# Kernel tuning notes

Measured on AMD Instinct MI355X. Metric: run time of the kernel, lower is better.

The kernel has to match this reference:

```python
import jax, jax.numpy as jnp
from jax import lax
import numpy as np

EPS = 1e-8


def _pdist(a):
    # torch.cdist(a, a, p=2): pairwise Euclidean distances [B, B]
    sq = jnp.sum(a * a, axis=1)
    d2 = sq[:, None] + sq[None, :] - 2.0 * (a @ a.T)
    d2 = jnp.maximum(d2, 0.0)
    # safe sqrt: zero distance -> 0 with zero (not NaN) gradient
    pos = d2 > 0
    return jnp.where(pos, jnp.sqrt(jnp.where(pos, d2, 1.0)), 0.0)


def _local_curvature(x, k):
    # PCA-residual curvature per sample: 1 - S0 / sum(S) over k-NN neighborhood
    dists = _pdist(x)                          # [B, B]
    _, knn_idx = lax.top_k(-dists, k + 1)      # smallest k+1 distances
    knn_idx = knn_idx[:, 1:]                   # drop self -> [B, k]
    nbrs = x[knn_idx]                          # [B, k, D] gather
    centered = nbrs - jnp.mean(nbrs, axis=1, keepdims=True)
    S = jnp.linalg.svd(centered, compute_uv=False)  # batched singular values [B, k]
    linearity = S[:, 0] / (jnp.sum(S, axis=1) + EPS)
    return 1.0 - linearity                     # [B]


def reference(z, ref_emb, x_original, k):
    B = z.shape[0]
    curv = _local_curvature(x_original, k)     # [B]
    z_dist = _pdist(z)
    ref_dist = _pdist(ref_emb)
    # weights = clamp(1 - max(curv_i, curv_j), min=0.1)
    weights = jnp.maximum(1.0 - jnp.maximum(curv[:, None], curv[None, :]), 0.1)
    z_norm = z_dist / (jnp.max(z_dist) + EPS)
    ref_norm = ref_dist / (jnp.max(ref_dist) + EPS)
    errors = (z_norm - ref_norm) ** 2 * weights
    mask = jnp.triu(jnp.ones((B, B), dtype=bool), k=1)
    n_pairs = B * (B - 1) / 2.0
    return jnp.sum(jnp.where(mask, errors, 0.0)) / n_pairs


def setup_inputs() -> dict:
    key = jax.random.key(0)
    k1, k2, k3 = jax.random.split(key, 3)
    B, D, DZ, DR = 4096, 1024, 128, 128
    return {
        "z": jax.random.normal(k1, (B, DZ), dtype=jnp.float32),
        "ref_emb": jax.random.normal(k2, (B, DR), dtype=jnp.float32),
        "x_original": jax.random.normal(k3, (B, D), dtype=jnp.float32),
        "k": 10,
    }
```

## Files before the change

### kernel.cpp

```cpp
#include <hip/hip_runtime.h>
#include <math.h>

#define NB 4096
#define DX 1024
#define DZ 128
#define KNN 10
#define STR 32
#define NLIST 32
#define BKK 64

typedef short short8v __attribute__((ext_vector_type(8)));
typedef float f32x4 __attribute__((ext_vector_type(4)));

#define MFMA16(a, b, c) __builtin_amdgcn_mfma_f32_16x16x32_bf16((a), (b), (c), 0, 0, 0)

__device__ __forceinline__ ushort f2bf(float f) {
  unsigned u = __float_as_uint(f);
  u += 0x7FFFu + ((u >> 16) & 1u);
  return (ushort)(u >> 16);
}
__device__ __forceinline__ float bf2f(ushort h) {
  return __uint_as_float(((unsigned)h) << 16);
}

__device__ __forceinline__ short8v frag_ld(const ushort* base, int row, int fg) {
  int off = (row << 6) + (fg << 4);
  off ^= (row & 7) << 4;
  return *(const short8v*)((const char*)base + off);
}

__device__ __forceinline__ int swz64(int row, int c8) {
  return (row << 7) + ((c8 ^ (row & 7)) << 4);
}
__device__ __forceinline__ short8v frag_ld64(const ushort* base, int row, int kk, int fg) {
  return *(const short8v*)((const char*)base + swz64(row, kk * 4 + fg));
}

#define INSERT10(td, ti, v, idx)                         \
  do {                                                   \
    if ((v) < td[KNN - 1]) {                             \
      _Pragma("unroll")                                  \
      for (int k_ = KNN - 1; k_ >= 1; --k_) {            \
        bool bk = (v) < td[k_];                          \
        bool bk1 = (v) < td[k_ - 1];                     \
        td[k_] = bk ? (bk1 ? td[k_ - 1] : (v)) : td[k_]; \
        ti[k_] = bk ? (bk1 ? ti[k_ - 1] : (idx)) : ti[k_]; \
      }                                                  \
      bool b0 = (v) < td[0];                             \
      ti[0] = b0 ? (idx) : ti[0];                        \
      td[0] = b0 ? (v) : td[0];                          \
    }                                                    \
  } while (0)

__global__ __launch_bounds__(256) void k_rowsq(const float* __restrict__ a,
                                               float* __restrict__ out, int D) {
  int row = blockIdx.x;
  const float4* p = (const float4*)(a + (size_t)row * D);
  float s = 0.f;
  for (int d = threadIdx.x; d < (D >> 2); d += 256) {
    float4 v = p[d];
    s = fmaf(v.x, v.x, s); s = fmaf(v.y, v.y, s);
    s = fmaf(v.z, v.z, s); s = fmaf(v.w, v.w, s);
  }
#pragma unroll
  for (int m = 32; m; m >>= 1) s += __shfl_xor(s, m);
  __shared__ float red[4];
  int w = threadIdx.x >> 6;
  if ((threadIdx.x & 63) == 0) red[w] = s;
  __syncthreads();
  if (threadIdx.x == 0) out[row] = red[0] + red[1] + red[2] + red[3];
}

__global__ __launch_bounds__(256) void k_prep_x(const float* __restrict__ x,
                                                ushort* __restrict__ xh,
                                                float* __restrict__ sqx) {
  const int row = blockIdx.x, t = threadIdx.x;
  float4 v = ((const float4*)(x + (size_t)row * DX))[t];
  ushort4 hv;
  hv.x = f2bf(v.x); hv.y = f2bf(v.y); hv.z = f2bf(v.z); hv.w = f2bf(v.w);
  ((ushort4*)(xh + (size_t)row * DX))[t] = hv;
  float s = fmaf(v.x, v.x, fmaf(v.y, v.y, fmaf(v.z, v.z, v.w * v.w)));
#pragma unroll
  for (int m = 32; m; m >>= 1) s += __shfl_xor(s, m);
  __shared__ float red[4];
  int w = t >> 6;
  if ((t & 63) == 0) red[w] = s;
  __syncthreads();
  if (t == 0) sqx[row] = red[0] + red[1] + red[2] + red[3];
}

__global__ __launch_bounds__(256) void k_prep_zr(const float* __restrict__ z,
                                                 const float* __restrict__ rfm,
                                                 ushort* __restrict__ zh, ushort* __restrict__ zl,
                                                 ushort* __restrict__ rh, ushort* __restrict__ rl,
                                                 float* __restrict__ sqz, float* __restrict__ sqr) {
  const float* src = blockIdx.y ? rfm : z;
  ushort* ph = blockIdx.y ? rh : zh;
  ushort* pl = blockIdx.y ? rl : zl;
  float* sq = blockIdx.y ? sqr : sqz;
  const int t = threadIdx.x;
  const size_t base = (size_t)blockIdx.x * 1024;
  float4 v = ((const float4*)(src + base))[t];
  float vv[4] = {v.x, v.y, v.z, v.w};
  ushort h[4], l[4];
#pragma unroll
  for (int e = 0; e < 4; ++e) {
    h[e] = f2bf(vv[e]);
    l[e] = f2bf(vv[e] - bf2f(h[e]));
  }
  ushort4 hv; hv.x = h[0]; hv.y = h[1]; hv.z = h[2]; hv.w = h[3];
  ushort4 lv; lv.x = l[0]; lv.y = l[1]; lv.z = l[2]; lv.w = l[3];
  ((ushort4*)(ph + base))[t] = hv;
  ((ushort4*)(pl + base))[t] = lv;
  float s = fmaf(v.x, v.x, fmaf(v.y, v.y, fmaf(v.z, v.z, v.w * v.w)));
#pragma unroll
  for (int m = 16; m; m >>= 1) s += __shfl_xor(s, m);
  if ((t & 31) == 0) sq[blockIdx.x * 8 + (t >> 5)] = s;
}

struct SmemKNN {
  union {
    struct { ushort A[256 * BKK], B[128 * BKK]; } s;
    float D[64 * 129];
  } u;
};

template<int PRE>
__global__ __launch_bounds__(512, 4) void k_knn(const float* __restrict__ x,
                                                const ushort* __restrict__ xh,
                                                const float* __restrict__ sqx,
                                                float* __restrict__ cand_d,
                                                int* __restrict__ cand_i) {
  __shared__ SmemKNN sm;
  const int bid = blockIdx.y * STR + blockIdx.x;
  const int xcd = bid & 7, rr = bid >> 3;
  const int strip = (xcd & 3) * 8 + (rr & 7);
  const int itile = (xcd >> 2) * 8 + (rr >> 3);
  const int i0 = itile * 256;
  const int j0 = strip * 128;

  const int tid = threadIdx.x;
  const int lane = tid & 63, wv = tid >> 6;
  const int wr = wv >> 1, wc = wv & 1;
  const int fr = lane & 15, fg = lane >> 4;

  float td[KNN];
  int ti[KNN];
#pragma unroll
  for (int k = 0; k < KNN; ++k) { td[k] = 3.0e38f; ti[k] = 0; }
  const int my_chunk = tid >> 7;
  const int t2 = tid & 127;
  const int srow = t2 >> 1;
  const int cbase = (tid & 1) * 64;

  f32x4 acc[4][4];
  const f32x4 zv4 = {0.f, 0.f, 0.f, 0.f};
#pragma unroll
  for (int m = 0; m < 4; ++m)
#pragma unroll
    for (int n = 0; n < 4; ++n) acc[m][n] = zv4;

  for (int kc = 0; kc < DX; kc += BKK) {
    __syncthreads();
    if (PRE) {
#pragma unroll
      for (int l = 0; l < 4; ++l) {
        int idx = tid + l * 512;
        int row = idx >> 3, c8 = idx & 7;
        *(uint4*)((char*)sm.u.s.A + swz64(row, c8)) =
            *(const uint4*)(xh + (size_t)(i0 + row) * DX + kc + c8 * 8);
      }
#pragma unroll
      for (int l = 0; l < 2; ++l) {
        int idx = tid + l * 512;
        int row = idx >> 3, c8 = idx & 7;
        *(uint4*)((char*)sm.u.s.B + swz64(row, c8)) =
            *(const uint4*)(xh + (size_t)(j0 + row) * DX + kc + c8 * 8);
      }
    } else {
#pragma unroll
      for (int l = 0; l < 4; ++l) {
        int idx = tid + l * 512;
        int row = idx >> 3, c8 = idx & 7;
        const float* pa = &x[(size_t)(i0 + row) * DX + kc + c8 * 8];
        float4 a1 = *(const float4*)pa, a2 = *(const float4*)(pa + 4);
        uint4 pva;
        pva.x = (unsigned)f2bf(a1.x) | ((unsigned)f2bf(a1.y) << 16);
        pva.y = (unsigned)f2bf(a1.z) | ((unsigned)f2bf(a1.w) << 16);
        pva.z = (unsigned)f2bf(a2.x) | ((unsigned)f2bf(a2.y) << 16);
        pva.w = (unsigned)f2bf(a2.z) | ((unsigned)f2bf(a2.w) << 16);
        *(uint4*)((char*)sm.u.s.A + swz64(row, c8)) = pva;
      }
#pragma unroll
      for (int l = 0; l < 2; ++l) {
        int idx = tid + l * 512;
        int row = idx >> 3, c8 = idx & 7;
        const float* pb = &x[(size_t)(j0 + row) * DX + kc + c8 * 8];
        float4 b1 = *(const float4*)pb, b2 = *(const float4*)(pb + 4);
        uint4 pvb;
        pvb.x = (unsigned)f2bf(b1.x) | ((unsigned)f2bf(b1.y) << 16);
        pvb.y = (unsigned)f2bf(b1.z) | ((unsigned)f2bf(b1.w) << 16);
        pvb.z = (unsigned)f2bf(b2.x) | ((unsigned)f2bf(b2.y) << 16);
        pvb.w = (unsigned)f2bf(b2.z) | ((unsigned)f2bf(b2.w) << 16);
        *(uint4*)((char*)sm.u.s.B + swz64(row, c8)) = pvb;
      }
    }
    __syncthreads();
#pragma unroll
    for (int kk = 0; kk < 2; ++kk) {
      short8v fa[4];
#pragma unroll
      for (int m = 0; m < 4; ++m)
        fa[m] = frag_ld64(sm.u.s.A, wr * 64 + m * 16 + fr, kk, fg);
#pragma unroll
      for (int n = 0; n < 4; ++n) {
        short8v fb = frag_ld64(sm.u.s.B, wc * 64 + n * 16 + fr, kk, fg);
#pragma unroll
        for (int m = 0; m < 4; ++m)
          acc[m][n] = MFMA16(fa[m], fb, acc[m][n]);
      }
    }
  }
  __syncthreads();
#pragma unroll
  for (int chunk = 0; chunk < 4; ++chunk) {
    if (wr == chunk) {
#pragma unroll
      for (int m = 0; m < 4; ++m)
#pragma unroll
        for (int n = 0; n < 4; ++n)
#pragma unroll
          for (int r = 0; r < 4; ++r) {
            int rl = m * 16 + fg * 4 + r;
            int cl = wc * 64 + n * 16 + fr;
            int gi = i0 + chunk * 64 + rl, gj = j0 + cl;
            float v = sqx[gi] + sqx[gj] - 2.f * acc[m][n][r];
            sm.u.D[rl * 129 + cl] = (gi == gj) ? 3.0e38f : v;
          }
    }
    __syncthreads();
    if (my_chunk == chunk) {
#pragma unroll 4
      for (int c = 0; c < 64; ++c) {
        float v = sm.u.D[srow * 129 + cbase + c];
        int idx = j0 + cbase + c;
        INSERT10(td, ti, v, idx);
      }
    }
    __syncthreads();
  }
  {
    float pd[KNN]; int pi[KNN];
#pragma unroll
    for (int l = 0; l < KNN; ++l) {
      pd[l] = __shfl_xor(td[l], 1);
      pi[l] = __shfl_xor(ti[l], 1);
    }
#pragma unroll
    for (int l = 0; l < KNN; ++l) INSERT10(td, ti, pd[l], pi[l]);
    if ((tid & 1) == 0) {
      int row = i0 + my_chunk * 64 + srow;
#pragma unroll
      for (int l = 0; l < KNN; ++l) {
        cand_d[((size_t)row * NLIST + strip) * KNN + l] = td[l];
        cand_i[((size_t)row * NLIST + strip) * KNN + l] = ti[l];
      }
    }
  }
}

template<int PRE>
__global__ __launch_bounds__(64) void k_mergegram(const float* __restrict__ cand_d,
                                                  const int* __restrict__ cand_i,
                                                  const float* __restrict__ x,
                                                  const ushort* __restrict__ xh,
                                                  float* __restrict__ G) {
  const int pt = blockIdx.x;
  const int lane = threadIdx.x;
  float v[KNN]; int jx[KNN];
  const float* cd = cand_d + ((size_t)pt * NLIST + lane) * KNN;
  const int* ci = cand_i + ((size_t)pt * NLIST + lane) * KNN;
  const bool act = lane < NLIST;
#pragma unroll
  for (int l = 0; l < KNN; ++l) {
    v[l] = act ? cd[l] : 3.0e38f;
    jx[l] = act ? ci[l] : 0;
  }
  int nbi[KNN];
#pragma unroll
  for (int k = 0; k < KNN; ++k) {
    float bv = v[0]; int bj = jx[0]; int bl = lane;
#pragma unroll
    for (int m = 1; m < 64; m <<= 1) {
      float ov = __shfl_xor(bv, m);
      int oj = __shfl_xor(bj, m);
      int ol = __shfl_xor(bl, m);
      bool take = ov < bv;
      bv = take ? ov : bv; bj = take ? oj : bj; bl = take ? ol : bl;
    }
    nbi[k] = bj;
    if (lane == bl) {
#pragma unroll
      for (int l = 0; l < KNN - 1; ++l) { v[l] = v[l + 1]; jx[l] = jx[l + 1]; }
      v[KNN - 1] = 3.0e38f;
    }
  }
  float P[55];
  float U[KNN];
  float q = 0.f;
#pragma unroll
  for (int c = 0; c < 55; ++c) P[c] = 0.f;
#pragma unroll
  for (int a = 0; a < KNN; ++a) U[a] = 0.f;
  if (PRE) {
    const short8v* nb[KNN];
#pragma unroll
    for (int a = 0; a < KNN; ++a)
      nb[a] = (const short8v*)(xh + (size_t)nbi[a] * DX);
    for (int d8 = lane; d8 < DX / 8; d8 += 64) {
      short8v n8[KNN];
#pragma unroll
      for (int a = 0; a < KNN; ++a) n8[a] = nb[a][d8];
#pragma unroll
      for (int e = 0; e < 8; ++e) {
        float n[KNN];
#pragma unroll
        for (int a = 0; a < KNN; ++a) n[a] = bf2f((ushort)n8[a][e]);
        float m = 0.f;
#pragma unroll
        for (int a = 0; a < KNN; ++a) m += n[a];
        m *= 0.1f;
        q = fmaf(m, m, q);
#pragma unroll
        for (int a = 0; a < KNN; ++a) U[a] = fmaf(n[a], m, U[a]);
        int c = 0;
#pragma unroll
        for (int a = 0; a < KNN; ++a)
#pragma unroll
          for (int b = a; b < KNN; ++b) { P[c] = fmaf(n[a], n[b], P[c]); ++c; }
      }
    }
  } else {
    const float4* nb[KNN];
#pragma unroll
    for (int a = 0; a < KNN; ++a)
      nb[a] = (const float4*)(x + (size_t)nbi[a] * DX);
    for (int d4 = lane; d4 < DX / 4; d4 += 64) {
      float4 n4[KNN];
#pragma unroll
      for (int a = 0; a < KNN; ++a) n4[a] = nb[a][d4];
#pragma unroll
      for (int e = 0; e < 4; ++e) {
        float n[KNN];
#pragma unroll
        for (int a = 0; a < KNN; ++a) n[a] = ((const float*)&n4[a])[e];
        float m = 0.f;
#pragma unroll
        for (int a = 0; a < KNN; ++a) m += n[a];
        m *= 0.1f;
        q = fmaf(m, m, q);
#pragma unroll
        for (int a = 0; a < KNN; ++a) U[a] = fmaf(n[a], m, U[a]);
        int c = 0;
#pragma unroll
        for (int a = 0; a < KNN; ++a)
#pragma unroll
          for (int b = a; b < KNN; ++b) { P[c] = fmaf(n[a], n[b], P[c]); ++c; }
      }
    }
  }
#pragma unroll
  for (int c = 0; c < 55; ++c)
#pragma unroll
    for (int m2 = 32; m2; m2 >>= 1) P[c] += __shfl_xor(P[c], m2);
#pragma unroll
  for (int a = 0; a < KNN; ++a)
#pragma unroll
    for (int m2 = 32; m2; m2 >>= 1) U[a] += __shfl_xor(U[a], m2);
#pragma unroll
  for (int m2 = 32; m2; m2 >>= 1) q += __shfl_xor(q, m2);
  if (lane == 0) {
    int c = 0;
    for (int a = 0; a < KNN; ++a)
      for (int b = a; b < KNN; ++b) { G[(size_t)pt * 55 + c] = P[c] - U[a] - U[b] + q; ++c; }
  }
}

__device__ __forceinline__ constexpr int IJ(int a, int b) {
  return (a <= b) ? (10 * a - (a * (a - 1)) / 2 + (b - a))
                  : (10 * b - (b * (b - 1)) / 2 + (a - b));
}

#define NSWEEP 6
__global__ __launch_bounds__(64) void k_jacobi(const float* __restrict__ G,
                                               float* __restrict__ curv) {
  const int pt = blockIdx.x * 64 + threadIdx.x;
  float M[55];
#pragma unroll
  for (int c = 0; c < 55; ++c) M[c] = G[(size_t)pt * 55 + c];

#pragma unroll
  for (int sweep = 0; sweep < NSWEEP; ++sweep) {
#pragma unroll
    for (int p = 0; p < KNN - 1; ++p) {
#pragma unroll
      for (int q = p + 1; q < KNN; ++q) {
        float apq = M[IJ(p, q)];
        float app = M[IJ(p, p)], aqq = M[IJ(q, q)];
        float theta = (aqq - app) / (2.f * apq);
        float t = 1.f / (fabsf(theta) + sqrtf(fmaf(theta, theta, 1.f)));
        t = (theta < 0.f) ? -t : t;
        t = (apq == 0.f) ? 0.f : t;
        float cc = 1.f / sqrtf(fmaf(t, t, 1.f));
        float ss = t * cc;
#pragma unroll
        for (int r = 0; r < KNN; ++r) {
          if (r == p || r == q) continue;
          float vrp = M[IJ(r, p)];
          float vrq = M[IJ(r, q)];
          M[IJ(r, p)] = cc * vrp - ss * vrq;
          M[IJ(r, q)] = ss * vrp + cc * vrq;
        }
        M[IJ(p, p)] = app - t * apq;
        M[IJ(q, q)] = aqq + t * apq;
        M[IJ(p, q)] = 0.f;
      }
    }
  }

  float lmax = 0.f, ssum = 0.f;
#pragma unroll
  for (int a = 0; a < KNN; ++a) {
    float l = fmaxf(M[IJ(a, a)], 0.f);
    lmax = fmaxf(lmax, l);
    ssum += sqrtf(l);
  }
  curv[pt] = 1.f - sqrtf(lmax) / (ssum + 1e-8f);
}

template<int PRE>
__global__ __launch_bounds__(256, 2) void k_zr(const float* __restrict__ z,
                                               const float* __restrict__ rfm,
                                               const ushort* __restrict__ zh,
                                               const ushort* __restrict__ zl,
                                               const ushort* __restrict__ rh,
                                               const ushort* __restrict__ rl,
                                               const float* __restrict__ sqz,
                                               const float* __restrict__ sqr,
                                               const float* __restrict__ curv,
                                               double* __restrict__ pS,
                                               float* __restrict__ pM) {
  __shared__ struct { ushort Ah[4096], Al[4096], Bh[4096], Bl[4096]; } s;
  const int t = blockIdx.x;
  int ib = 0, base = 0;
  while (base + (32 - ib) <= t) { base += 32 - ib; ++ib; }
  const int jb = ib + (t - base);
  const int i0 = ib * 128, j0 = jb * 128;
  const int tid = threadIdx.x;
  const int lane = tid & 63, wv = tid >> 6;
  const int wr = wv >> 1, wc = wv & 1;
  const int fr = lane & 15, fg = lane >> 4;

  f32x4 zacc[4][4], racc[4][4];
  const f32x4 zv = {0.f, 0.f, 0.f, 0.f};
#pragma unroll
  for (int m = 0; m < 4; ++m)
#pragma unroll
    for (int n = 0; n < 4; ++n) { zacc[m][n] = zv; racc[m][n] = zv; }

#pragma unroll
  for (int mat = 0; mat < 2; ++mat) {
    const float* P = mat ? rfm : z;
    const ushort* Ph = mat ? rh : zh;
    const ushort* Pl = mat ? rl : zl;
    for (int kc = 0; kc < DZ; kc += 32) {
      __syncthreads();
      if (PRE) {
#pragma unroll
        for (int l = 0; l < 2; ++l) {
          int idx = tid + l * 256;
          int row = idx >> 2, c8 = idx & 3;
          int off = (row << 6) + (c8 << 4);
          off ^= (row & 7) << 4;
          size_t ga = (size_t)(i0 + row) * DZ + kc + c8 * 8;
          size_t gb = (size_t)(j0 + row) * DZ + kc + c8 * 8;
          *(uint4*)((char*)s.Ah + off) = *(const uint4*)(Ph + ga);
          *(uint4*)((char*)s.Al + off) = *(const uint4*)(Pl + ga);
          *(uint4*)((char*)s.Bh + off) = *(const uint4*)(Ph + gb);
          *(uint4*)((char*)s.Bl + off) = *(const uint4*)(Pl + gb);
        }
      } else {
#pragma unroll
        for (int l = 0; l < 4; ++l) {
          int idx = tid + l * 256;
          int row = idx >> 3, c4 = idx & 7;
          int off = (row << 6) + (c4 << 3);
          off ^= (row & 7) << 4;
          float4 va = *(const float4*)&P[(size_t)(i0 + row) * DZ + kc + c4 * 4];
          float4 vb = *(const float4*)&P[(size_t)(j0 + row) * DZ + kc + c4 * 4];
          float av[4] = {va.x, va.y, va.z, va.w};
          float bv[4] = {vb.x, vb.y, vb.z, vb.w};
          ushort ah4[4], al4[4], bh4[4], bl4[4];
#pragma unroll
          for (int e = 0; e < 4; ++e) {
            ah4[e] = f2bf(av[e]); al4[e] = f2bf(av[e] - bf2f(ah4[e]));
            bh4[e] = f2bf(bv[e]); bl4[e] = f2bf(bv[e] - bf2f(bh4[e]));
          }
          uint2 p;
          p.x = (unsigned)ah4[0] | ((unsigned)ah4[1] << 16);
          p.y = (unsigned)ah4[2] | ((unsigned)ah4[3] << 16);
          *(uint2*)((char*)s.Ah + off) = p;
          p.x = (unsigned)al4[0] | ((unsigned)al4[1] << 16);
          p.y = (unsigned)al4[2] | ((unsigned)al4[3] << 16);
          *(uint2*)((char*)s.Al + off) = p;
          p.x = (unsigned)bh4[0] | ((unsigned)bh4[1] << 16);
          p.y = (unsigned)bh4[2] | ((unsigned)bh4[3] << 16);
          *(uint2*)((char*)s.Bh + off) = p;
          p.x = (unsigned)bl4[0] | ((unsigned)bl4[1] << 16);
          p.y = (unsigned)bl4[2] | ((unsigned)bl4[3] << 16);
          *(uint2*)((char*)s.Bl + off) = p;
        }
      }
      __syncthreads();
      short8v fah[4], fal[4];
#pragma unroll
      for (int m = 0; m < 4; ++m) {
        int r = wr * 64 + m * 16 + fr;
        fah[m] = frag_ld(s.Ah, r, fg);
        fal[m] = frag_ld(s.Al, r, fg);
      }
#pragma unroll
      for (int n = 0; n < 4; ++n) {
        int r = wc * 64 + n * 16 + fr;
        short8v fbh = frag_ld(s.Bh, r, fg);
        short8v fbl = frag_ld(s.Bl, r, fg);
#pragma unroll
        for (int m = 0; m < 4; ++m) {
          if (mat == 0) {
            zacc[m][n] = MFMA16(fah[m], fbh, zacc[m][n]);
            zacc[m][n] = MFMA16(fah[m], fbl, zacc[m][n]);
            zacc[m][n] = MFMA16(fal[m], fbh, zacc[m][n]);
          } else {
            racc[m][n] = MFMA16(fah[m], fbh, racc[m][n]);
            racc[m][n] = MFMA16(fah[m], fbl, racc[m][n]);
            racc[m][n] = MFMA16(fal[m], fbh, racc[m][n]);
          }
        }
      }
    }
  }

  double s1 = 0, s2 = 0, s3 = 0;
  float mz = 0.f, mr = 0.f;
#pragma unroll
  for (int m = 0; m < 4; ++m)
#pragma unroll
    for (int n = 0; n < 4; ++n)
#pragma unroll
      for (int r = 0; r < 4; ++r) {
        int gi = i0 + wr * 64 + m * 16 + fg * 4 + r;
        int gj = j0 + wc * 64 + n * 16 + fr;
        if (gj > gi) {
          float z2 = fmaxf(sqz[gi] + sqz[gj] - 2.f * zacc[m][n][r], 0.f);
          float r2 = fmaxf(sqr[gi] + sqr[gj] - 2.f * racc[m][n][r], 0.f);
          float w = fmaxf(1.f - fmaxf(curv[gi], curv[gj]), 0.1f);
          s1 += (double)(w * z2);
          s3 += (double)(w * r2);
          s2 += (double)(w * sqrtf(z2 * r2));
          mz = fmaxf(mz, z2);
          mr = fmaxf(mr, r2);
        }
      }
#pragma unroll
  for (int m = 32; m; m >>= 1) {
    s1 += __shfl_xor(s1, m);
    s2 += __shfl_xor(s2, m);
    s3 += __shfl_xor(s3, m);
    mz = fmaxf(mz, __shfl_xor(mz, m));
    mr = fmaxf(mr, __shfl_xor(mr, m));
  }
  __shared__ double rd[4][3];
  __shared__ float rf2[4][2];
  int w = tid >> 6;
  if ((tid & 63) == 0) { rd[w][0] = s1; rd[w][1] = s2; rd[w][2] = s3; rf2[w][0] = mz; rf2[w][1] = mr; }
  __syncthreads();
  if (tid == 0) {
    double a = 0, b = 0, c = 0; float d = 0.f, e = 0.f;
    for (int i = 0; i < 4; ++i) {
      a += rd[i][0]; b += rd[i][1]; c += rd[i][2];
      d = fmaxf(d, rf2[i][0]); e = fmaxf(e, rf2[i][1]);
    }
    pS[(size_t)t * 3 + 0] = a; pS[(size_t)t * 3 + 1] = b; pS[(size_t)t * 3 + 2] = c;
    pM[(size_t)t * 2 + 0] = d; pM[(size_t)t * 2 + 1] = e;
  }
}

__global__ __launch_bounds__(256) void k_final(const double* __restrict__ pS,
                                               const float* __restrict__ pM,
                                               int nb, float* __restrict__ out) {
  int tid = threadIdx.x;
  double s1 = 0, s2 = 0, s3 = 0; float mz = 0.f, mr = 0.f;
  for (int i = tid; i < nb; i += 256) {
    s1 += pS[(size_t)i * 3 + 0]; s2 += pS[(size_t)i * 3 + 1]; s3 += pS[(size_t)i * 3 + 2];
    mz = fmaxf(mz, pM[(size_t)i * 2 + 0]); mr = fmaxf(mr, pM[(size_t)i * 2 + 1]);
  }
#pragma unroll
  for (int m = 32; m; m >>= 1) {
    s1 += __shfl_xor(s1, m); s2 += __shfl_xor(s2, m); s3 += __shfl_xor(s3, m);
    mz = fmaxf(mz, __shfl_xor(mz, m)); mr = fmaxf(mr, __shfl_xor(mr, m));
  }
  __shared__ double rd[4][3];
  __shared__ float rf2[4][2];
  int w = tid >> 6;
  if ((tid & 63) == 0) { rd[w][0] = s1; rd[w][1] = s2; rd[w][2] = s3; rf2[w][0] = mz; rf2[w][1] = mr; }
  __syncthreads();
  if (tid == 0) {
    double a = 0, b = 0, c = 0; float d = 0.f, e = 0.f;
    for (int i = 0; i < 4; ++i) {
      a += rd[i][0]; b += rd[i][1]; c += rd[i][2];
      d = fmaxf(d, rf2[i][0]); e = fmaxf(e, rf2[i][1]);
    }
    double zm = sqrt((double)d) + 1e-8;
    double rm = sqrt((double)e) + 1e-8;
    double total = a / (zm * zm) - 2.0 * b / (zm * rm) + c / (rm * rm);
    double npairs = (double)NB * (double)(NB - 1) / 2.0;
    out[0] = (float)(total / npairs);
  }
}

extern "C" void kernel_launch(void* const* d_in, const int* in_sizes, int n_in,
                              void* d_out, int out_size, void* d_ws, size_t ws_size,
                              hipStream_t stream) {
  const float* z = (const float*)d_in[0];
  const float* rfm = (const float*)d_in[1];
  const float* x = (const float*)d_in[2];
  float* out = (float*)d_out;
  char* w = (char*)d_ws;

  float*  sqx    = (float*)(w + 0);
  float*  sqz    = (float*)(w + 16384);
  float*  sqr    = (float*)(w + 32768);
  float*  curv   = (float*)(w + 49152);
  float*  cand_d = (float*)(w + 229376);
  int*    cand_i = (int*)(w + 5472256);
  float*  G      = (float*)(w + 10715136);
  double* pS     = (double*)(w + 11616256);
  float*  pM     = (float*)(w + 11628928);

  ushort* xh = (ushort*)(w + (size_t)12 * 1024 * 1024);
  ushort* zh = (ushort*)(w + (size_t)20 * 1024 * 1024);
  ushort* zl = (ushort*)(w + (size_t)21 * 1024 * 1024);
  ushort* rh = (ushort*)(w + (size_t)22 * 1024 * 1024);
  ushort* rl = (ushort*)(w + (size_t)23 * 1024 * 1024);
  const bool pre = ws_size >= (size_t)24 * 1024 * 1024;

  if (pre) {
    k_prep_x<<<NB, 256, 0, stream>>>(x, xh, sqx);
    k_prep_zr<<<dim3(NB * DZ / 1024, 2), 256, 0, stream>>>(z, rfm, zh, zl, rh, rl, sqz, sqr);
    k_knn<1><<<dim3(STR, NB / 256), 512, 0, stream>>>(x, xh, sqx, cand_d, cand_i);
    k_mergegram<1><<<NB, 64, 0, stream>>>(cand_d, cand_i, x, xh, G);
  } else {
    k_rowsq<<<NB, 256, 0, stream>>>(x, sqx, DX);
    k_rowsq<<<NB, 256, 0, stream>>>(z, sqz, DZ);
    k_rowsq<<<NB, 256, 0, stream>>>(rfm, sqr, DZ);
    k_knn<0><<<dim3(STR, NB / 256), 512, 0, stream>>>(x, xh, sqx, cand_d, cand_i);
    k_mergegram<0><<<NB, 64, 0, stream>>>(cand_d, cand_i, x, xh, G);
  }
  k_jacobi<<<NB / 64, 64, 0, stream>>>(G, curv);
  if (pre) {
    k_zr<1><<<528, 256, 0, stream>>>(z, rfm, zh, zl, rh, rl, sqz, sqr, curv, pS, pM);
  } else {
    k_zr<0><<<528, 256, 0, stream>>>(z, rfm, zh, zl, rh, rl, sqz, sqr, curv, pS, pM);
  }
  k_final<<<1, 256, 0, stream>>>(pS, pM, 528, out);
}
```

Before: 267.6 us.

## Exploit distance-matrix symmetry in kNN by computing only upper-triangular tiles

The kNN Gram kernel now launches 528 blocks of 128x128 tiles over the upper triangle (ib<=jb) instead of the full 4096x4096 product. For off-diagonal tiles each block also scans its tile column-wise, building top-10 candidates for the j rows, and writes them into the (j, ib) slot of the candidate list. This roughly halves the MFMA and global load work of the dominant GEMM. In exchange it adds a second column-wise insertion pass, an extra shared-memory exchange, and a more uneven workload per block, with blocks shrunk from 512 to 256 threads.

```diff
diff --git a/kernel.cpp b/kernel.cpp
--- a/kernel.cpp
+++ b/kernel.cpp
@@ -5,7 +5,7 @@
 #define DX 1024
 #define DZ 128
 #define KNN 10
-#define STR 32
+#define NTILE 32
 #define NLIST 32
 #define BKK 64
 
@@ -120,39 +120,31 @@
 
 struct SmemKNN {
   union {
-    struct { ushort A[256 * BKK], B[128 * BKK]; } s;
+    struct { ushort A[128 * BKK], B[128 * BKK]; } s;
     float D[64 * 129];
   } u;
 };
 
 template<int PRE>
-__global__ __launch_bounds__(512, 4) void k_knn(const float* __restrict__ x,
+__global__ __launch_bounds__(256, 4) void k_knn(const float* __restrict__ x,
                                                 const ushort* __restrict__ xh,
                                                 const float* __restrict__ sqx,
                                                 float* __restrict__ cand_d,
                                                 int* __restrict__ cand_i) {
   __shared__ SmemKNN sm;
-  const int bid = blockIdx.y * STR + blockIdx.x;
-  const int xcd = bid & 7, rr = bid >> 3;
-  const int strip = (xcd & 3) * 8 + (rr & 7);
-  const int itile = (xcd >> 2) * 8 + (rr >> 3);
-  const int i0 = itile * 256;
-  const int j0 = strip * 128;
+  const int bt = (blockIdx.x & 7) * 66 + (blockIdx.x >> 3);
+  int ib = 0, base = 0;
+  while (base + (NTILE - ib) <= bt) { base += NTILE - ib; ++ib; }
+  const int jb = ib + (bt - base);
+  const int i0 = ib * 128;
+  const int j0 = jb * 128;
+  const bool diag = (ib == jb);
 
   const int tid = threadIdx.x;
   const int lane = tid & 63, wv = tid >> 6;
   const int wr = wv >> 1, wc = wv & 1;
   const int fr = lane & 15, fg = lane >> 4;
 
-  float td[KNN];
-  int ti[KNN];
-#pragma unroll
-  for (int k = 0; k < KNN; ++k) { td[k] = 3.0e38f; ti[k] = 0; }
-  const int my_chunk = tid >> 7;
-  const int t2 = tid & 127;
-  const int srow = t2 >> 1;
-  const int cbase = (tid & 1) * 64;
-
   f32x4 acc[4][4];
   const f32x4 zv4 = {0.f, 0.f, 0.f, 0.f};
 #pragma unroll
@@ -165,44 +157,35 @@
     if (PRE) {
 #pragma unroll
       for (int l = 0; l < 4; ++l) {
-        int idx = tid + l * 512;
+        int idx = tid + l * 256;
         int row = idx >> 3, c8 = idx & 7;
-        *(uint4*)((char*)sm.u.s.A + swz64(row, c8)) =
+        int off = swz64(row, c8);
+        *(uint4*)((char*)sm.u.s.A + off) =
             *(const uint4*)(xh + (size_t)(i0 + row) * DX + kc + c8 * 8);
-      }
-#pragma unroll
-      for (int l = 0; l < 2; ++l) {
-        int idx = tid + l * 512;
+        *(uint4*)((char*)sm.u.s.B + off) =
+            *(const uint4*)(xh + (size_t)(j0 + row) * DX + kc + c8 * 8);
+      }
+    } else {
+#pragma unroll
+      for (int l = 0; l < 4; ++l) {
+        int idx = tid + l * 256;
         int row = idx >> 3, c8 = idx & 7;
-        *(uint4*)((char*)sm.u.s.B + swz64(row, c8)) =
-            *(const uint4*)(xh + (size_t)(j0 + row) * DX + kc + c8 * 8);
-      }
-    } else {
-#pragma unroll
-      for (int l = 0; l < 4; ++l) {
-        int idx = tid + l * 512;
-        int row = idx >> 3, c8 = idx & 7;
+        int off = swz64(row, c8);
         const float* pa = &x[(size_t)(i0 + row) * DX + kc + c8 * 8];
+        const float* pb = &x[(size_t)(j0 + row) * DX + kc + c8 * 8];
         float4 a1 = *(const float4*)pa, a2 = *(const float4*)(pa + 4);
-        uint4 pva;
+        float4 b1 = *(const float4*)pb, b2 = *(const float4*)(pb + 4);
+        uint4 pva, pvb;
         pva.x = (unsigned)f2bf(a1.x) | ((unsigned)f2bf(a1.y) << 16);
         pva.y = (unsigned)f2bf(a1.z) | ((unsigned)f2bf(a1.w) << 16);
         pva.z = (unsigned)f2bf(a2.x) | ((unsigned)f2bf(a2.y) << 16);
         pva.w = (unsigned)f2bf(a2.z) | ((unsigned)f2bf(a2.w) << 16);
-        *(uint4*)((char*)sm.u.s.A + swz64(row, c8)) = pva;
-      }
-#pragma unroll
-      for (int l = 0; l < 2; ++l) {
-        int idx = tid + l * 512;
-        int row = idx >> 3, c8 = idx & 7;
-        const float* pb = &x[(size_t)(j0 + row) * DX + kc + c8 * 8];
-        float4 b1 = *(const float4*)pb, b2 = *(const float4*)(pb + 4);
-        uint4 pvb;
         pvb.x = (unsigned)f2bf(b1.x) | ((unsigned)f2bf(b1.y) << 16);
         pvb.y = (unsigned)f2bf(b1.z) | ((unsigned)f2bf(b1.w) << 16);
         pvb.z = (unsigned)f2bf(b2.x) | ((unsigned)f2bf(b2.y) << 16);
         pvb.w = (unsigned)f2bf(b2.z) | ((unsigned)f2bf(b2.w) << 16);
-        *(uint4*)((char*)sm.u.s.B + swz64(row, c8)) = pvb;
+        *(uint4*)((char*)sm.u.s.A + off) = pva;
+        *(uint4*)((char*)sm.u.s.B + off) = pvb;
       }
     }
     __syncthreads();
@@ -222,8 +205,18 @@
     }
   }
   __syncthreads();
-#pragma unroll
-  for (int chunk = 0; chunk < 4; ++chunk) {
+
+  float td[KNN]; int ti[KNN];
+  float tc[KNN]; int tjx[KNN];
+#pragma unroll
+  for (int k = 0; k < KNN; ++k) { td[k] = 3.0e38f; ti[k] = 0; tc[k] = 3.0e38f; tjx[k] = 0; }
+  const int grp = tid >> 7;
+  const int t2 = tid & 127;
+  const int srow = t2 >> 1;
+  const int cbase = (tid & 1) * 64;
+
+#pragma unroll
+  for (int chunk = 0; chunk < 2; ++chunk) {
     if (wr == chunk) {
 #pragma unroll
       for (int m = 0; m < 4; ++m)
@@ -239,13 +232,20 @@
           }
     }
     __syncthreads();
-    if (my_chunk == chunk) {
+    if (grp == chunk) {
 #pragma unroll 4
       for (int c = 0; c < 64; ++c) {
         float v = sm.u.D[srow * 129 + cbase + c];
         int idx = j0 + cbase + c;
         INSERT10(td, ti, v, idx);
       }
+    } else if (!diag) {
+#pragma unroll 4
+      for (int r = 0; r < 64; ++r) {
+        float v = sm.u.D[r * 129 + t2];
+        int idx = i0 + chunk * 64 + r;
+        INSERT10(tc, tjx, v, idx);
+      }
     }
     __syncthreads();
   }
@@ -259,11 +259,37 @@
 #pragma unroll
     for (int l = 0; l < KNN; ++l) INSERT10(td, ti, pd[l], pi[l]);
     if ((tid & 1) == 0) {
-      int row = i0 + my_chunk * 64 + srow;
+      int row = i0 + grp * 64 + srow;
 #pragma unroll
       for (int l = 0; l < KNN; ++l) {
-        cand_d[((size_t)row * NLIST + strip) * KNN + l] = td[l];
-        cand_i[((size_t)row * NLIST + strip) * KNN + l] = ti[l];
+        cand_d[((size_t)row * NLIST + jb) * KNN + l] = td[l];
+        cand_i[((size_t)row * NLIST + jb) * KNN + l] = ti[l];
+      }
+    }
+  }
+  if (!diag) {
+    float* exd = sm.u.D;
+    int* exi = (int*)sm.u.D;
+    if (grp == 1) {
+#pragma unroll
+      for (int l = 0; l < KNN; ++l) {
+        exd[t2 * 20 + l] = tc[l];
+        exi[t2 * 20 + 10 + l] = tjx[l];
+      }
+    }
+    __syncthreads();
+    if (grp == 0) {
+#pragma unroll
+      for (int l = 0; l < KNN; ++l) {
+        float v = exd[t2 * 20 + l];
+        int j = exi[t2 * 20 + 10 + l];
+        INSERT10(tc, tjx, v, j);
+      }
+      int row = j0 + t2;
+#pragma unroll
+      for (int l = 0; l < KNN; ++l) {
+        cand_d[((size_t)row * NLIST + ib) * KNN + l] = tc[l];
+        cand_i[((size_t)row * NLIST + ib) * KNN + l] = tjx[l];
       }
     }
   }
@@ -657,13 +683,13 @@
   if (pre) {
     k_prep_x<<<NB, 256, 0, stream>>>(x, xh, sqx);
     k_prep_zr<<<dim3(NB * DZ / 1024, 2), 256, 0, stream>>>(z, rfm, zh, zl, rh, rl, sqz, sqr);
-    k_knn<1><<<dim3(STR, NB / 256), 512, 0, stream>>>(x, xh, sqx, cand_d, cand_i);
+    k_knn<1><<<528, 256, 0, stream>>>(x, xh, sqx, cand_d, cand_i);
     k_mergegram<1><<<NB, 64, 0, stream>>>(cand_d, cand_i, x, xh, G);
   } else {
     k_rowsq<<<NB, 256, 0, stream>>>(x, sqx, DX);
     k_rowsq<<<NB, 256, 0, stream>>>(z, sqz, DZ);
     k_rowsq<<<NB, 256, 0, stream>>>(rfm, sqr, DZ);
-    k_knn<0><<<dim3(STR, NB / 256), 512, 0, stream>>>(x, xh, sqx, cand_d, cand_i);
+    k_knn<0><<<528, 256, 0, stream>>>(x, xh, sqx, cand_d, cand_i);
     k_mergegram<0><<<NB, 64, 0, stream>>>(cand_d, cand_i, x, xh, G);
   }
   k_jacobi<<<NB / 64, 64, 0, stream>>>(G, curv);
```

Measured after the change: 276.2 us. 1.03x slower.
